# Performance work log

Hardware: AMD Instinct MI355X
Metric: run time of the kernel (lower is better)

## Reference

```python
import jax, jax.numpy as jnp
import numpy as np

UNITS = 1024
HORIZON = 24
FEATURES = 128


def _lstm_gates(xt, h, c, W, U, b):
    # Keras gate order: i, f, g(candidate), o; activation=tanh, recurrent_activation=sigmoid
    z = xt @ W + h @ U + b  # [B, 4U]
    i, f, g, o = jnp.split(z, 4, axis=-1)
    c_new = jax.nn.sigmoid(f) * c + jax.nn.sigmoid(i) * jnp.tanh(g)
    h_new = jax.nn.sigmoid(o) * jnp.tanh(c_new)
    return h_new, c_new


def setup_inputs() -> dict:
    key = jax.random.key(0)
    ks = jax.random.split(key, 9)
    s = 0.05
    return {
        "x": jax.random.normal(ks[0], (256, 512, FEATURES), dtype=jnp.float32),
        "enc_W": jax.random.normal(ks[1], (FEATURES, 4 * UNITS), dtype=jnp.float32) * s,
        "enc_U": jax.random.normal(ks[2], (UNITS, 4 * UNITS), dtype=jnp.float32) * s,
        "enc_b": jnp.zeros((4 * UNITS,), dtype=jnp.float32),
        "cell_W": jax.random.normal(ks[3], (UNITS, 4 * UNITS), dtype=jnp.float32) * s,
        "cell_U": jax.random.normal(ks[4], (UNITS, 4 * UNITS), dtype=jnp.float32) * s,
        "cell_b": jnp.zeros((4 * UNITS,), dtype=jnp.float32),
        "dense_W": jax.random.normal(ks[5], (UNITS, 1), dtype=jnp.float32) * s,
        "dense_b": jnp.zeros((1,), dtype=jnp.float32),
    }


def reference(x, enc_W, enc_U, enc_b, cell_W, cell_U, cell_b, dense_W, dense_b):
    B = x.shape[0]
    h0 = jnp.zeros((B, UNITS), dtype=x.dtype)
    c0 = jnp.zeros((B, UNITS), dtype=x.dtype)

    # Encoder LSTM (return_state): scan over time, keep final h, c
    def enc_step(carry, xt):
        h, c = carry
        h, c = _lstm_gates(xt, h, c, enc_W, enc_U, enc_b)
        return (h, c), None

    (h_enc, c_enc), _ = jax.lax.scan(enc_step, (h0, c0), jnp.swapaxes(x, 0, 1))

    def dec_step(carry, _):
        x_in, h, c = carry
        h, c = _lstm_gates(x_in, h, c, cell_W, cell_U, cell_b)
        pred = h @ dense_W + dense_b  # [B, 1]
        return (h, h, c), pred

    _, preds = jax.lax.scan(dec_step, (h_enc, h_enc, c_enc), None, length=HORIZON)
    # preds: [horizon, B, 1] -> [B, horizon, 1]
    return jnp.transpose(preds, (1, 0, 2))
```

## Files before the change

kernel.cpp:

```cpp
#include <hip/hip_runtime.h>
#include <cstdint>

#define NWG  256
#define NTHR 512
#define HBUF_U64 65536ull
#define WS_NEED  (HBUF_U64 * 2ull * 8ull + 1024ull)
#define BLDS_BYTES 147456
#define SMEM_BYTES (BLDS_BYTES + 16384)

typedef __attribute__((ext_vector_type(8))) short  short8;
typedef __attribute__((ext_vector_type(4))) float  float4v;
typedef unsigned long long u64;

#define ALD(p)    __hip_atomic_load((p), __ATOMIC_RELAXED, __HIP_MEMORY_SCOPE_AGENT)
#define AST(p, v) __hip_atomic_store((p), (v), __ATOMIC_RELAXED, __HIP_MEMORY_SCOPE_AGENT)

__device__ __forceinline__ short bf16r(float f) {
  union { float f; uint32_t u; } v; v.f = f;
  uint32_t r = (v.u + 0x7FFFu + ((v.u >> 16) & 1u)) >> 16;
  return (short)(uint16_t)r;
}
__device__ __forceinline__ float sig_(float x)  { return 1.f / (1.f + __expf(-x)); }
__device__ __forceinline__ float tanh_(float x) {
  x = fminf(15.f, fmaxf(-15.f, x));
  float e = __expf(-2.f * x);
  return (1.f - e) / (1.f + e);
}

__device__ __forceinline__ unsigned mall_load(const unsigned* p) {
  unsigned v;
  asm volatile("global_load_dword %0, %1, off sc0 sc1\n\t"
               "s_waitcnt vmcnt(0)"
               : "=v"(v) : "v"((unsigned long long)p) : "memory");
  return v;
}
__device__ __forceinline__ void mall_store(unsigned* p, unsigned v) {
  asm volatile("global_store_dword %0, %1, off sc0 sc1"
               :: "v"((unsigned long long)p), "v"(v) : "memory");
}

__global__ void __launch_bounds__(NTHR, 1)
lstm_all(const float* __restrict__ x,
         const float* __restrict__ encW, const float* __restrict__ encU, const float* __restrict__ encB,
         const float* __restrict__ celW, const float* __restrict__ celU, const float* __restrict__ celB,
         const float* __restrict__ denW, const float* __restrict__ denB,
         float* __restrict__ out,
         u64* __restrict__ hb, unsigned* __restrict__ barp)
{
  extern __shared__ char smem[];
  float* zs = (float*)(smem + BLDS_BYTES);

  const int tid = threadIdx.x, wg = blockIdx.x;
  const int wgr = (wg & 7) >> 1;
  const int wgc = ((wg >> 3) << 1) | (wg & 1);
  unsigned* bar = barp + wgr * 64;
  unsigned syncno = 0;

  if (tid < 256)
    AST(hb + (size_t)wgc * 1024 + (size_t)wgr * 256 + tid, 0ull);
  if (wgc == 0)
    for (int i = tid; i < 768; i += NTHR)
      AST((u64*)out + (size_t)wgr * 768 + i, 0ull);

  {
    const int r = tid & 63, slot = tid >> 6;
    const int n = (r >> 4) * 1024 + wgc * 16 + (r & 15);
    for (int i = 0; i < 5; ++i) {
      int kk = slot + 8 * i;
      if (kk < 36) {
        for (int j8 = 0; j8 < 4; ++j8) {
          short8 v;
#pragma unroll
          for (int j = 0; j < 8; ++j) {
            int k = kk * 32 + j8 * 8 + j;
            float f = (k < 128) ? encW[(size_t)k * 4096 + n]
                                : encU[(size_t)(k - 128) * 4096 + n];
            v[j] = bf16r(f);
          }
          uint32_t byte = ((uint32_t)(r * 1152 + kk * 32 + j8 * 8) * 2u) ^ (uint32_t)((r & 7) << 4);
          *(short8*)(smem + byte) = v;
        }
      }
    }
  }

  const int lane = tid & 63, wv = tid >> 6;
  const int l15 = lane & 15, lq = lane >> 4;
  const int mq = wv & 1, ks = wv >> 1;
  uint32_t bbase[4], bmask[4];
#pragma unroll
  for (int nf = 0; nf < 4; ++nf) {
    int rB = nf * 16 + l15;
    bbase[nf] = (uint32_t)((rB * 1152 + lq * 8) * 2);
    bmask[nf] = (uint32_t)((rB & 7) << 4);
  }
  const int erow = tid >> 3, ecp = tid & 7;
  const int gcol0 = wgc * 16 + 2 * ecp, gcol1 = gcol0 + 1;
  const int growg = wgr * 64 + erow;
  const int erot  = ((erow >> 2) & 3) << 4;
  const float bei0 = encB[gcol0], bei1 = encB[gcol1];
  const float bef0 = encB[1024 + gcol0], bef1 = encB[1024 + gcol1];
  const float beg0 = encB[2048 + gcol0], beg1 = encB[2048 + gcol1];
  const float beo0 = encB[3072 + gcol0], beo1 = encB[3072 + gcol1];
  const float bci0 = celB[gcol0], bci1 = celB[gcol1];
  const float bcf0 = celB[1024 + gcol0], bcf1 = celB[1024 + gcol1];
  const float bcg0 = celB[2048 + gcol0], bcg1 = celB[2048 + gcol1];
  const float bco0 = celB[3072 + gcol0], bco1 = celB[3072 + gcol1];
  const float dw0 = denW[gcol0], dw1 = denW[gcol1], db = denB[0];
  float cA = 0.f, cB = 0.f;
  int cur = 0;
  float4v acc[2][4];

  auto xpart = [&](int t) {
    const int Kg = ks * 32;
    const float* xp0 = x + ((size_t)(wgr * 64 + mq * 32 + l15) * 512 + (size_t)t) * 128 + Kg + lq * 8;
    const float* xp1 = xp0 + (size_t)16 * 512 * 128;
    float4v u0 = *(const float4v*)xp0, u1 = *(const float4v*)(xp0 + 4);
    float4v w0 = *(const float4v*)xp1, w1 = *(const float4v*)(xp1 + 4);
    short8 a0, a1;
#pragma unroll
    for (int j = 0; j < 4; ++j) {
      a0[j] = bf16r(u0[j]); a0[4 + j] = bf16r(u1[j]);
      a1[j] = bf16r(w0[j]); a1[4 + j] = bf16r(w1[j]);
    }
#pragma unroll
    for (int nf = 0; nf < 4; ++nf) {
      short8 b = *(const short8*)(smem + ((bbase[nf] + 2u * (uint32_t)Kg) ^ bmask[nf]));
      acc[0][nf] = __builtin_amdgcn_mfma_f32_16x16x32_bf16(a0, b, acc[0][nf], 0, 0, 0);
      acc[1][nf] = __builtin_amdgcn_mfma_f32_16x16x32_bf16(a1, b, acc[1][nf], 0, 0, 0);
    }
  };

  auto hpart = [&](const u64* hbase, int wk0) {
    const int rbase = wgr * 64 + mq * 32 + l15;
    u64 q0[8], q1[8], q2[8], q3[8];
#pragma unroll
    for (int kk = 0; kk < 8; ++kk) {
      const int kc = ks * 256 + kk * 32;
      const int c0 = kc + lq * 8;
      const size_t bidx = (size_t)(c0 >> 4) * 1024 + (size_t)rbase * 4 + (size_t)((c0 & 15) >> 2);
      q0[kk] = ALD(hbase + bidx);
      q1[kk] = ALD(hbase + bidx + 1);
      q2[kk] = ALD(hbase + bidx + 64);
      q3[kk] = ALD(hbase + bidx + 65);
    }
#pragma unroll
    for (int kk = 0; kk < 8; ++kk) {
      const int kc = ks * 256 + kk * 32;
      union { u64 q[2]; short8 s; } ua, ub;
      ua.q[0] = q0[kk]; ua.q[1] = q1[kk];
      ub.q[0] = q2[kk]; ub.q[1] = q3[kk];
      const uint32_t Kw = (uint32_t)(wk0 + kc);
#pragma unroll
      for (int nf = 0; nf < 4; ++nf) {
        short8 b = *(const short8*)(smem + ((bbase[nf] + 2u * Kw) ^ bmask[nf]));
        acc[0][nf] = __builtin_amdgcn_mfma_f32_16x16x32_bf16(ua.s, b, acc[0][nf], 0, 0, 0);
        acc[1][nf] = __builtin_amdgcn_mfma_f32_16x16x32_bf16(ub.s, b, acc[1][nf], 0, 0, 0);
      }
    }
  };

  auto reduce_zs = [&]() {
#pragma unroll
    for (int mf = 0; mf < 2; ++mf)
#pragma unroll
      for (int nf = 0; nf < 4; ++nf)
#pragma unroll
        for (int e = 0; e < 4; ++e) {
          int row = mq * 32 + mf * 16 + lq * 4 + e;
          int col = (nf * 16 + l15) ^ (lq << 4);
          atomicAdd(&zs[row * 64 + col], acc[mf][nf][e]);
        }
  };

  auto st_reload = [&]() {
    const int r = tid & 63, slot = tid >> 6;
    const int n = (r >> 4) * 1024 + wgc * 16 + (r & 15);
    for (int i = 0; i < 4; ++i) {
      int kk = slot + 8 * i;
      for (int j8 = 0; j8 < 4; ++j8) {
        short8 v;
#pragma unroll
        for (int j = 0; j < 8; ++j) {
          int k = kk * 32 + j8 * 8 + j;
          float f = celW[(size_t)k * 4096 + n] + celU[(size_t)k * 4096 + n];
          v[j] = bf16r(f);
        }
        uint32_t byte = ((uint32_t)(r * 1152 + kk * 32 + j8 * 8) * 2u) ^ (uint32_t)((r & 7) << 4);
        *(short8*)(smem + byte) = v;
      }
    }
  };

  auto barrier_overlap = [&](int xt, bool reload) {
    asm volatile("s_waitcnt vmcnt(0)" ::: "memory");
    __syncthreads();
    ++syncno;
    if (tid == 0) mall_store(bar + wgc, syncno);
    { float* p = zs + tid * 8; float4v zz = {0.f,0.f,0.f,0.f};
      *(float4v*)p = zz; *(float4v*)(p + 4) = zz; }
#pragma unroll
    for (int mf = 0; mf < 2; ++mf)
#pragma unroll
      for (int nf = 0; nf < 4; ++nf) acc[mf][nf] = (float4v){0.f,0.f,0.f,0.f};
    if (xt >= 0) xpart(xt);
    if (reload) st_reload();
    if (tid < 64) {
      while (mall_load(bar + tid) < syncno)
        __builtin_amdgcn_s_sleep(4);
    }
    __syncthreads();
  };

  auto epilogue = [&](bool dec, int td) {
    const float* zr = zs + erow * 64;
    float2 I = *(const float2*)(zr + (( 0 + 2 * ecp) ^ erot));
    float2 F = *(const float2*)(zr + ((16 + 2 * ecp) ^ erot));
    float2 G = *(const float2*)(zr + ((32 + 2 * ecp) ^ erot));
    float2 O = *(const float2*)(zr + ((48 + 2 * ecp) ^ erot));
    float i0, i1, f0, f1, g0, g1, o0, o1;
    if (!dec) { i0=I.x+bei0; i1=I.y+bei1; f0=F.x+bef0; f1=F.y+bef1;
                g0=G.x+beg0; g1=G.y+beg1; o0=O.x+beo0; o1=O.y+beo1; }
    else      { i0=I.x+bci0; i1=I.y+bci1; f0=F.x+bcf0; f1=F.y+bcf1;
                g0=G.x+bcg0; g1=G.y+bcg1; o0=O.x+bco0; o1=O.y+bco1; }
    cA = sig_(f0) * cA + sig_(i0) * tanh_(g0);
    cB = sig_(f1) * cB + sig_(i1) * tanh_(g1);
    float hA = sig_(o0) * tanh_(cA);
    float hB = sig_(o1) * tanh_(cB);
    unsigned hp = (unsigned)(unsigned short)bf16r(hA)
                | ((unsigned)(unsigned short)bf16r(hB) << 16);
    unsigned* h32 = (unsigned*)hb;
    size_t idx = (size_t)(cur ^ 1) * 131072 + (size_t)wgc * 2048 + (size_t)growg * 8 + ecp;
    AST(h32 + idx, hp);
    if (dec) {
      float p = hA * dw0 + hB * dw1;
      p += __shfl_xor(p, 1); p += __shfl_xor(p, 2); p += __shfl_xor(p, 4);
      if (ecp == 0)
        atomicAdd(&out[(size_t)growg * 24 + td], p + (wgc == 0 ? db : 0.f));
    }
  };

  barrier_overlap(0, false);
  for (int t = 0; t < 512; ++t) {
    hpart(hb + (size_t)cur * HBUF_U64, 128);
    reduce_zs();
    __syncthreads();
    epilogue(false, 0);
    cur ^= 1;
    if (t < 511) barrier_overlap(t + 1, false);
    else         barrier_overlap(-1, true);
  }
  for (int td = 0; td < 24; ++td) {
    hpart(hb + (size_t)cur * HBUF_U64, 0);
    reduce_zs();
    __syncthreads();
    epilogue(true, td);
    cur ^= 1;
    if (td < 23) barrier_overlap(-1, false);
  }
}

extern "C" void kernel_launch(void* const* d_in, const int* in_sizes, int n_in,
                              void* d_out, int out_size, void* d_ws, size_t ws_size,
                              hipStream_t stream) {
  const float* x    = (const float*)d_in[0];
  const float* encW = (const float*)d_in[1];
  const float* encU = (const float*)d_in[2];
  const float* encB = (const float*)d_in[3];
  const float* celW = (const float*)d_in[4];
  const float* celU = (const float*)d_in[5];
  const float* celB = (const float*)d_in[6];
  const float* denW = (const float*)d_in[7];
  const float* denB = (const float*)d_in[8];
  float* out = (float*)d_out;

  if (ws_size < WS_NEED) return;

  u64*      hb  = (u64*)d_ws;
  unsigned* bar = (unsigned*)((char*)d_ws + HBUF_U64 * 2ull * 8ull);

  hipMemsetAsync(bar, 0, 1024, stream);
  hipFuncSetAttribute((const void*)lstm_all,
                      hipFuncAttributeMaxDynamicSharedMemorySize, SMEM_BYTES);

  void* args[] = { (void*)&x, (void*)&encW, (void*)&encU, (void*)&encB,
                   (void*)&celW, (void*)&celU, (void*)&celB,
                   (void*)&denW, (void*)&denB,
                   (void*)&out, (void*)&hb, (void*)&bar };
  hipLaunchCooperativeKernel((void*)lstm_all, dim3(NWG), dim3(NTHR), args,
                             (unsigned)SMEM_BYTES, stream);
}
```

Before: 13.95 ms.

## Replace persistent cooperative kernel with per-timestep launches and prepacked bf16 weights

Adds a new path used whenever the workspace is large enough. A prep kernel converts and swizzles the encoder and decoder weights to bf16 in global memory. Then one kernel is launched per timestep (512 encoder plus 24 decoder launches), each refilling its LDS weight slice with global_load_lds. This replaces the software grid barrier with kernel boundaries, but adds launch overhead and reloads about 147KB of weights into LDS on every step instead of keeping them resident. The old persistent kernel stays as a fallback.

```diff
diff --git a/kernel.cpp b/kernel.cpp
--- a/kernel.cpp
+++ b/kernel.cpp
@@ -1,19 +1,9 @@
 #include <hip/hip_runtime.h>
 #include <cstdint>
-
-#define NWG  256
-#define NTHR 512
-#define HBUF_U64 65536ull
-#define WS_NEED  (HBUF_U64 * 2ull * 8ull + 1024ull)
-#define BLDS_BYTES 147456
-#define SMEM_BYTES (BLDS_BYTES + 16384)
 
 typedef __attribute__((ext_vector_type(8))) short  short8;
 typedef __attribute__((ext_vector_type(4))) float  float4v;
 typedef unsigned long long u64;
-
-#define ALD(p)    __hip_atomic_load((p), __ATOMIC_RELAXED, __HIP_MEMORY_SCOPE_AGENT)
-#define AST(p, v) __hip_atomic_store((p), (v), __ATOMIC_RELAXED, __HIP_MEMORY_SCOPE_AGENT)
 
 __device__ __forceinline__ short bf16r(float f) {
   union { float f; uint32_t u; } v; v.f = f;
@@ -26,6 +16,199 @@
   float e = __expf(-2.f * x);
   return (1.f - e) / (1.f + e);
 }
+
+#define WREG_BYTES 9437184ull
+#define HB_BYTES   1048576ull
+#define CB_BYTES   1048576ull
+#define NEED_STEP  (WREG_BYTES + HB_BYTES + CB_BYTES)
+
+__global__ void prep_zero(u64* hb, u64* cc, u64* outw) {
+  int g = blockIdx.x * 256 + threadIdx.x;
+#pragma unroll
+  for (int i = 0; i < 8; ++i) hb[g + i * 16384] = 0ull;
+#pragma unroll
+  for (int i = 0; i < 8; ++i) cc[g + i * 16384] = 0ull;
+  if (g < 768) outw[g] = 0ull;
+}
+
+__global__ void prep_weights(const float* __restrict__ A, const float* __restrict__ B,
+                             short* __restrict__ dst, int KW, int enc) {
+  __shared__ short tl[64][68];
+  const int kt = blockIdx.x >> 6, nt = blockIdx.x & 63;
+  const int tid = threadIdx.x;
+  const int kl = tid >> 6, nl = tid & 63;
+  for (int r = 0; r < 16; ++r) {
+    int k = kt * 64 + r * 4 + kl, n = nt * 64 + nl;
+    float f;
+    if (enc) f = (k < 128) ? A[(size_t)k * 4096 + n] : B[(size_t)(k - 128) * 4096 + n];
+    else     f = A[(size_t)k * 4096 + n] + B[(size_t)k * 4096 + n];
+    tl[r * 4 + kl][nl] = bf16r(f);
+  }
+  __syncthreads();
+  for (int i = 0; i < 4; ++i) {
+    int idx = i * 256 + tid;
+    int nl2 = idx >> 4, k4 = idx & 15;
+    int n = nt * 64 + nl2, kb = k4 * 4;
+    short4 v;
+    v.x = tl[kb][nl2]; v.y = tl[kb + 1][nl2]; v.z = tl[kb + 2][nl2]; v.w = tl[kb + 3][nl2];
+    uint32_t byterow = (uint32_t)(kt * 64 + kb) * 2u;
+    size_t off = (size_t)n * (size_t)(KW * 2) + (size_t)(byterow ^ (uint32_t)((n & 7) << 4));
+    *(short4*)((char*)dst + off) = v;
+  }
+}
+
+template<int KW, int DEC>
+__global__ void __launch_bounds__(512, 1)
+lstm_step(const float* __restrict__ x, int t, const short* __restrict__ Wt,
+          const u64* __restrict__ hsrc, u64* __restrict__ hdst,
+          float* __restrict__ cst, const float* __restrict__ bias,
+          const float* __restrict__ denW, const float* __restrict__ denB,
+          float* __restrict__ out, int td)
+{
+  extern __shared__ char smem[];
+  float* zs = (float*)(smem + KW * 128);
+  const int tid = threadIdx.x, wg = blockIdx.x;
+  const int wgc = wg & 63, wgr = wg >> 6;
+  const int lane = tid & 63, wv = tid >> 6;
+  const int l15 = lane & 15, lq = lane >> 4;
+  const int mq = wv & 1, ks = wv >> 1;
+
+  {
+    constexpr int NCH = (KW * 128) / 8192;
+    for (int i = 0; i < NCH; ++i) {
+      uint32_t base = (uint32_t)((i * 8 + wv) * 1024);
+      uint32_t ldsoff = base + (uint32_t)lane * 16u;
+      uint32_t rB = ldsoff / (uint32_t)(KW * 2);
+      uint32_t koff = ldsoff - rB * (uint32_t)(KW * 2);
+      uint32_t n = (rB >> 4) * 1024u + (uint32_t)wgc * 16u + (rB & 15u);
+      const char* src = (const char*)Wt + (size_t)n * (size_t)(KW * 2) + koff;
+      __builtin_amdgcn_global_load_lds(
+          (const __attribute__((address_space(1))) void*)src,
+          (__attribute__((address_space(3))) void*)(smem + base), 16, 0, 0);
+    }
+  }
+
+  float4v u0, u1, w0, w1;
+  if constexpr (!DEC) {
+    const float* xp0 = x + ((size_t)(wgr * 64 + mq * 32 + l15) * 512 + (size_t)t) * 128 + ks * 32 + lq * 8;
+    const float* xp1 = xp0 + (size_t)16 * 512 * 128;
+    u0 = *(const float4v*)xp0; u1 = *(const float4v*)(xp0 + 4);
+    w0 = *(const float4v*)xp1; w1 = *(const float4v*)(xp1 + 4);
+  }
+  u64 q0[8], q1[8], q2[8], q3[8];
+  {
+    const char* hr0 = (const char*)hsrc + (size_t)(wgr * 64 + mq * 32 + l15) * 2048;
+    const char* hr1 = hr0 + 16 * 2048;
+#pragma unroll
+    for (int kk = 0; kk < 8; ++kk) {
+      uint32_t kb = (uint32_t)(ks * 256 + kk * 32 + lq * 8) * 2u;
+      q0[kk] = *(const u64*)(hr0 + kb); q1[kk] = *(const u64*)(hr0 + kb + 8);
+      q2[kk] = *(const u64*)(hr1 + kb); q3[kk] = *(const u64*)(hr1 + kb + 8);
+    }
+  }
+  const int erow = tid >> 3, ecp = tid & 7;
+  const int gcol0 = wgc * 16 + 2 * ecp, gcol1 = gcol0 + 1;
+  const int growg = wgr * 64 + erow;
+  const int erot = ((erow >> 2) & 3) << 4;
+  const float bi0 = bias[gcol0],        bi1 = bias[gcol1];
+  const float bf0 = bias[1024 + gcol0], bf1 = bias[1024 + gcol1];
+  const float bg0 = bias[2048 + gcol0], bg1 = bias[2048 + gcol1];
+  const float bo0 = bias[3072 + gcol0], bo1 = bias[3072 + gcol1];
+  float2 cc = *(const float2*)(cst + (size_t)growg * 1024 + gcol0);
+  float dw0 = 0.f, dw1 = 0.f, db = 0.f;
+  if constexpr (DEC) { dw0 = denW[gcol0]; dw1 = denW[gcol1]; db = denB[0]; }
+
+  { float* p = zs + tid * 8; float4v z = {0.f,0.f,0.f,0.f};
+    *(float4v*)p = z; *(float4v*)(p + 4) = z; }
+
+  asm volatile("s_waitcnt vmcnt(0)" ::: "memory");
+  __syncthreads();
+
+  uint32_t bbase[4], bmask[4];
+#pragma unroll
+  for (int nf = 0; nf < 4; ++nf) {
+    int rB = nf * 16 + l15;
+    bbase[nf] = (uint32_t)((rB * KW + lq * 8) * 2);
+    bmask[nf] = (uint32_t)((rB & 7) << 4);
+  }
+  float4v acc[2][4];
+#pragma unroll
+  for (int a = 0; a < 2; ++a)
+#pragma unroll
+    for (int b = 0; b < 4; ++b) acc[a][b] = (float4v){0.f,0.f,0.f,0.f};
+
+  if constexpr (!DEC) {
+    short8 a0, a1;
+#pragma unroll
+    for (int j = 0; j < 4; ++j) {
+      a0[j] = bf16r(u0[j]); a0[4 + j] = bf16r(u1[j]);
+      a1[j] = bf16r(w0[j]); a1[4 + j] = bf16r(w1[j]);
+    }
+    const uint32_t Kg = (uint32_t)(ks * 32);
+#pragma unroll
+    for (int nf = 0; nf < 4; ++nf) {
+      short8 b = *(const short8*)(smem + ((bbase[nf] + 2u * Kg) ^ bmask[nf]));
+      acc[0][nf] = __builtin_amdgcn_mfma_f32_16x16x32_bf16(a0, b, acc[0][nf], 0, 0, 0);
+      acc[1][nf] = __builtin_amdgcn_mfma_f32_16x16x32_bf16(a1, b, acc[1][nf], 0, 0, 0);
+    }
+  }
+#pragma unroll
+  for (int kk = 0; kk < 8; ++kk) {
+    union { u64 q[2]; short8 s; } ua, ub;
+    ua.q[0] = q0[kk]; ua.q[1] = q1[kk];
+    ub.q[0] = q2[kk]; ub.q[1] = q3[kk];
+    const uint32_t Kw = (uint32_t)((DEC ? 0 : 128) + ks * 256 + kk * 32);
+#pragma unroll
+    for (int nf = 0; nf < 4; ++nf) {
+      short8 b = *(const short8*)(smem + ((bbase[nf] + 2u * Kw) ^ bmask[nf]));
+      acc[0][nf] = __builtin_amdgcn_mfma_f32_16x16x32_bf16(ua.s, b, acc[0][nf], 0, 0, 0);
+      acc[1][nf] = __builtin_amdgcn_mfma_f32_16x16x32_bf16(ub.s, b, acc[1][nf], 0, 0, 0);
+    }
+  }
+#pragma unroll
+  for (int mf = 0; mf < 2; ++mf)
+#pragma unroll
+    for (int nf = 0; nf < 4; ++nf)
+#pragma unroll
+      for (int e = 0; e < 4; ++e) {
+        int row = mq * 32 + mf * 16 + lq * 4 + e;
+        int col = (nf * 16 + l15) ^ (lq << 4);
+        atomicAdd(&zs[row * 64 + col], acc[mf][nf][e]);
+      }
+  __syncthreads();
+
+  {
+    const float* zr = zs + erow * 64;
+    float2 I = *(const float2*)(zr + (( 0 + 2 * ecp) ^ erot));
+    float2 F = *(const float2*)(zr + ((16 + 2 * ecp) ^ erot));
+    float2 G = *(const float2*)(zr + ((32 + 2 * ecp) ^ erot));
+    float2 O = *(const float2*)(zr + ((48 + 2 * ecp) ^ erot));
+    float cA = sig_(F.x + bf0) * cc.x + sig_(I.x + bi0) * tanh_(G.x + bg0);
+    float cB = sig_(F.y + bf1) * cc.y + sig_(I.y + bi1) * tanh_(G.y + bg1);
+    float hA = sig_(O.x + bo0) * tanh_(cA);
+    float hB = sig_(O.y + bo1) * tanh_(cB);
+    *(float2*)(cst + (size_t)growg * 1024 + gcol0) = make_float2(cA, cB);
+    unsigned hp = (unsigned)(unsigned short)bf16r(hA)
+                | ((unsigned)(unsigned short)bf16r(hB) << 16);
+    ((unsigned*)hdst)[(size_t)growg * 512 + wgc * 8 + ecp] = hp;
+    if constexpr (DEC) {
+      float p = hA * dw0 + hB * dw1;
+      p += __shfl_xor(p, 1); p += __shfl_xor(p, 2); p += __shfl_xor(p, 4);
+      if (ecp == 0)
+        atomicAdd(&out[(size_t)growg * 24 + td], p + (wgc == 0 ? db : 0.f));
+    }
+  }
+}
+
+#define NWG  256
+#define NTHR 512
+#define HBUF_U64 65536ull
+#define WS_NEED_FB (HBUF_U64 * 2ull * 8ull + 1024ull)
+#define BLDS_BYTES 147456
+#define SMEM_BYTES (BLDS_BYTES + 16384)
+
+#define ALD(p)    __hip_atomic_load((p), __ATOMIC_RELAXED, __HIP_MEMORY_SCOPE_AGENT)
+#define AST(p, v) __hip_atomic_store((p), (v), __ATOMIC_RELAXED, __HIP_MEMORY_SCOPE_AGENT)
 
 __device__ __forceinline__ unsigned mall_load(const unsigned* p) {
   unsigned v;
@@ -49,7 +232,6 @@
 {
   extern __shared__ char smem[];
   float* zs = (float*)(smem + BLDS_BYTES);
-
   const int tid = threadIdx.x, wg = blockIdx.x;
   const int wgr = (wg & 7) >> 1;
   const int wgc = ((wg >> 3) << 1) | (wg & 1);
@@ -83,7 +265,6 @@
       }
     }
   }
-
   const int lane = tid & 63, wv = tid >> 6;
   const int l15 = lane & 15, lq = lane >> 4;
   const int mq = wv & 1, ks = wv >> 1;
@@ -130,7 +311,6 @@
       acc[1][nf] = __builtin_amdgcn_mfma_f32_16x16x32_bf16(a1, b, acc[1][nf], 0, 0, 0);
     }
   };
-
   auto hpart = [&](const u64* hbase, int wk0) {
     const int rbase = wgr * 64 + mq * 32 + l15;
     u64 q0[8], q1[8], q2[8], q3[8];
@@ -139,10 +319,8 @@
       const int kc = ks * 256 + kk * 32;
       const int c0 = kc + lq * 8;
       const size_t bidx = (size_t)(c0 >> 4) * 1024 + (size_t)rbase * 4 + (size_t)((c0 & 15) >> 2);
-      q0[kk] = ALD(hbase + bidx);
-      q1[kk] = ALD(hbase + bidx + 1);
-      q2[kk] = ALD(hbase + bidx + 64);
-      q3[kk] = ALD(hbase + bidx + 65);
+      q0[kk] = ALD(hbase + bidx);      q1[kk] = ALD(hbase + bidx + 1);
+      q2[kk] = ALD(hbase + bidx + 64); q3[kk] = ALD(hbase + bidx + 65);
     }
 #pragma unroll
     for (int kk = 0; kk < 8; ++kk) {
@@ -159,7 +337,6 @@
       }
     }
   };
-
   auto reduce_zs = [&]() {
 #pragma unroll
     for (int mf = 0; mf < 2; ++mf)
@@ -172,7 +349,6 @@
           atomicAdd(&zs[row * 64 + col], acc[mf][nf][e]);
         }
   };
-
   auto st_reload = [&]() {
     const int r = tid & 63, slot = tid >> 6;
     const int n = (r >> 4) * 1024 + wgc * 16 + (r & 15);
@@ -191,7 +367,6 @@
       }
     }
   };
-
   auto barrier_overlap = [&](int xt, bool reload) {
     asm volatile("s_waitcnt vmcnt(0)" ::: "memory");
     __syncthreads();
@@ -206,12 +381,10 @@
     if (xt >= 0) xpart(xt);
     if (reload) st_reload();
     if (tid < 64) {
-      while (mall_load(bar + tid) < syncno)
-        __builtin_amdgcn_s_sleep(4);
+      while (mall_load(bar + tid) < syncno) __builtin_amdgcn_s_sleep(4);
     }
     __syncthreads();
   };
-
   auto epilogue = [&](bool dec, int td) {
     const float* zr = zs + erow * 64;
     float2 I = *(const float2*)(zr + (( 0 + 2 * ecp) ^ erot));
@@ -274,15 +447,42 @@
   const float* denB = (const float*)d_in[8];
   float* out = (float*)d_out;
 
-  if (ws_size < WS_NEED) return;
-
+  if (ws_size >= NEED_STEP) {
+    short* Wt  = (short*)d_ws;
+    u64*   hbw = (u64*)((char*)d_ws + WREG_BYTES);
+    float* cst = (float*)((char*)d_ws + WREG_BYTES + HB_BYTES);
+    const size_t HBUF = 65536;
+
+    hipFuncSetAttribute((const void*)lstm_step<1152,0>,
+                        hipFuncAttributeMaxDynamicSharedMemorySize, 163840);
+    hipFuncSetAttribute((const void*)lstm_step<1024,1>,
+                        hipFuncAttributeMaxDynamicSharedMemorySize, 163840);
+
+    prep_zero<<<64, 256, 0, stream>>>(hbw, (u64*)cst, (u64*)out);
+    prep_weights<<<18 * 64, 256, 0, stream>>>(encW, encU, Wt, 1152, 1);
+    for (int t = 0; t < 512; ++t) {
+      const u64* hs = hbw + (size_t)(t & 1) * HBUF;
+      u64*       hd = hbw + (size_t)((t + 1) & 1) * HBUF;
+      lstm_step<1152,0><<<256, 512, 163840, stream>>>(
+          x, t, Wt, hs, hd, cst, encB, nullptr, nullptr, nullptr, 0);
+    }
+    prep_weights<<<16 * 64, 256, 0, stream>>>(celW, celU, Wt, 1024, 0);
+    for (int td = 0; td < 24; ++td) {
+      int cur = td & 1;
+      const u64* hs = hbw + (size_t)cur * HBUF;
+      u64*       hd = hbw + (size_t)(cur ^ 1) * HBUF;
+      lstm_step<1024,1><<<256, 512, 163840, stream>>>(
+          nullptr, 0, Wt, hs, hd, cst, celB, denW, denB, out, td);
+    }
+    return;
+  }
+
+  if (ws_size < WS_NEED_FB) return;
   u64*      hb  = (u64*)d_ws;
   unsigned* bar = (unsigned*)((char*)d_ws + HBUF_U64 * 2ull * 8ull);
-
   hipMemsetAsync(bar, 0, 1024, stream);
   hipFuncSetAttribute((const void*)lstm_all,
                       hipFuncAttributeMaxDynamicSharedMemorySize, SMEM_BYTES);
-
   void* args[] = { (void*)&x, (void*)&encW, (void*)&encU, (void*)&encB,
                    (void*)&celW, (void*)&celU, (void*)&celB,
                    (void*)&denW, (void*)&denB,
```

Measured after the change: 17.29 ms. 23.9% more time.
